# Kernel tuning notes

Measured on AMD Instinct MI355X. Metric: run time of the kernel, lower is better.

Reference implementation:

```python
import jax, jax.numpy as jnp
import numpy as np

SOS = 4998
EOS = 4999
SCALING = 2.0


def setup_inputs() -> dict:
    key = jax.random.key(0)
    ks = jax.random.split(key, 12)
    B, T, E, D, A, C, F, ODIM, L = 32, 1000, 512, 1024, 512, 10, 100, 5000, 100
    s = 0.02
    return {
        "hpad": jax.random.normal(ks[0], (B, T, E), jnp.float32),
        "ys": jax.random.randint(ks[1], (B, L), 0, SOS, jnp.int32),
        # AttLoc params
        "w_enc": jax.random.normal(ks[2], (A, E), jnp.float32) * s,
        "b_enc": jnp.zeros((A,), jnp.float32),
        "w_dec": jax.random.normal(ks[3], (A, D), jnp.float32) * s,
        "w_att": jax.random.normal(ks[4], (A, C), jnp.float32) * s,
        "w_conv": jax.random.normal(ks[5], (C, 1, 2 * F + 1), jnp.float32) * s,  # OIH 1D conv kernel
        "w_gvec": jax.random.normal(ks[6], (1, A), jnp.float32) * s,
        "b_gvec": jnp.zeros((1,), jnp.float32),
        # Decoder params
        "embed": jax.random.normal(ks[7], (ODIM, D), jnp.float32) * s,
        "w_ih": jax.random.normal(ks[8], (4 * D, D + E), jnp.float32) * s,
        "w_hh": jax.random.normal(ks[9], (4 * D, D), jnp.float32) * s,
        "b_ih": jnp.zeros((4 * D,), jnp.float32),
        "b_hh": jnp.zeros((4 * D,), jnp.float32),
        "w_out": jax.random.normal(ks[10], (ODIM, D), jnp.float32) * s,
        "b_out": jnp.zeros((ODIM,), jnp.float32),
    }


def _decode(hpad, ys, w_enc, b_enc, w_dec, w_att, w_conv, w_gvec, b_gvec,
            embed, w_ih, w_hh, b_ih, b_hh, w_out, b_out):
    B, T, E = hpad.shape
    D = w_hh.shape[1]
    F = (w_conv.shape[-1] - 1) // 2
    # ys_in = [sos; y] per utterance (all same length -> already padded)
    ys_in = jnp.concatenate([jnp.full((B, 1), SOS, ys.dtype), ys], axis=1)  # [B, olen]
    eys = embed[ys_in]                                                      # [B, olen, D]
    # pre_compute_enc_h = mlp_enc(enc_h)
    pre = jnp.einsum('bte,ae->bta', hpad, w_enc) + b_enc                    # [B, T, A]
    att0 = jnp.full((B, T), 1.0 / T, hpad.dtype)   # uniform init attention (all hlen == T)
    z0 = jnp.zeros((B, D), hpad.dtype)
    c0 = jnp.zeros((B, D), hpad.dtype)

    def step(carry, ey_i):
        z, c, aw = carry
        # location-aware conv over previous attention weights: [B,1,T] -> [B,C,T]
        conv = jax.lax.conv_general_dilated(aw[:, None, :], w_conv, (1,), [(F, F)],
                                            dimension_numbers=('NCH', 'OIH', 'NCH'))
        att_feat = jnp.einsum('bct,ac->bta', conv, w_att)                   # mlp_att
        dec = (z @ w_dec.T)[:, None, :]                                     # mlp_dec, tiled
        e = jnp.tanh(att_feat + pre + dec) @ w_gvec[0] + b_gvec[0]          # [B, T]
        w = jax.nn.softmax(SCALING * e, axis=1)
        ctx = jnp.einsum('bt,bte->be', w, hpad)                             # [B, E]
        # LSTMCell
        x = jnp.concatenate([ey_i, ctx], axis=1)                            # [B, D+E]
        gates = x @ w_ih.T + b_ih + z @ w_hh.T + b_hh
        i_g, f_g, g_g, o_g = jnp.split(gates, 4, axis=1)
        c_new = jax.nn.sigmoid(f_g) * c + jax.nn.sigmoid(i_g) * jnp.tanh(g_g)
        z_new = jax.nn.sigmoid(o_g) * jnp.tanh(c_new)
        return (z_new, c_new, w), z_new

    _, z_all = jax.lax.scan(step, (z0, c0, att0), jnp.swapaxes(eys, 0, 1))  # [olen, B, D]
    y_all = jnp.einsum('obd,vd->obv', z_all, w_out) + b_out                 # [olen, B, odim]
    return jnp.swapaxes(y_all, 0, 1)                                        # [B, olen, odim]


def reference(hpad, ys, w_enc, b_enc, w_dec, w_att, w_conv, w_gvec, b_gvec,
              embed, w_ih, w_hh, b_ih, b_hh, w_out, b_out):
    return _decode(hpad, ys, w_enc, b_enc, w_dec, w_att, w_conv, w_gvec, b_gvec,
                   embed, w_ih, w_hh, b_ih, b_hh, w_out, b_out)
```

## Files before the change

kernel.cpp:

```cpp
#include <hip/hip_runtime.h>
#include <math.h>

#define B_    32
#define T_    1000
#define E_    512
#define D_    1024
#define A_    512
#define C_    10
#define F_    100
#define ODIM_ 5000
#define OLEN_ 101
#define SOS_  4998

#define OFF_PRE   0u
#define N_PRE     (32u*1000u*512u)
#define OFF_DEC   (OFF_PRE + N_PRE)
#define N_DEC     (32u*512u)
#define OFF_CONV  (OFF_DEC + N_DEC)
#define N_CONVB   (32u*10u*1000u)
#define OFF_EB    (OFF_CONV + N_CONVB)
#define N_EB      (32u*1000u)
#define OFF_AW    (OFF_EB + N_EB)
#define OFF_CTX   (OFF_AW + N_EB)
#define N_CTX     (32u*512u)
#define OFF_GP    (OFF_CTX + N_CTX)
#define N_GP      (10u*32u*4096u)
#define OFF_Z     (OFF_GP + N_GP)
#define N_Z       (32u*1024u)
#define OFF_C     (OFF_Z + N_Z)
#define OFF_ZALL  (OFF_C + N_Z)

__device__ __forceinline__ float fast_tanh(float x) {
    float cx = fminf(8.f, fmaxf(-8.f, x));
    float e = __expf(2.f * cx);
    return (e - 1.f) * __builtin_amdgcn_rcpf(e + 1.f);
}
__device__ __forceinline__ float fast_sigmoid(float x) {
    float cx = fminf(30.f, fmaxf(-30.f, x));
    return __builtin_amdgcn_rcpf(1.f + __expf(-cx));
}

__global__ __launch_bounds__(256) void k_init(float* ws) {
    int i = blockIdx.x * 256 + threadIdx.x;
    if (i < (int)N_Z) { ws[OFF_Z + i] = 0.f; ws[OFF_C + i] = 0.f; }
    if (i < (int)N_EB) ws[OFF_AW + i] = 1.0f / (float)T_;
}

__global__ __launch_bounds__(256) void k_pre(const float* __restrict__ hp,
                                             const float* __restrict__ we,
                                             const float* __restrict__ be,
                                             float* __restrict__ pre) {
    __shared__ float As[64][68];
    __shared__ float Bs[64][68];
    int m0 = blockIdx.y * 64, n0 = blockIdx.x * 64;
    int tid = threadIdx.x;
    int tr = tid >> 4, tc = tid & 15;
    float acc[4][4] = {};
    for (int k0 = 0; k0 < 512; k0 += 64) {
        for (int i = tid; i < 1024; i += 256) {
            int m = i >> 4, kq = (i & 15) << 2;
            float4 v = *(const float4*)&hp[(size_t)(m0 + m) * 512 + k0 + kq];
            As[kq + 0][m] = v.x; As[kq + 1][m] = v.y; As[kq + 2][m] = v.z; As[kq + 3][m] = v.w;
            float4 w = *(const float4*)&we[(size_t)(n0 + m) * 512 + k0 + kq];
            Bs[kq + 0][m] = w.x; Bs[kq + 1][m] = w.y; Bs[kq + 2][m] = w.z; Bs[kq + 3][m] = w.w;
        }
        __syncthreads();
        #pragma unroll 16
        for (int kk = 0; kk < 64; ++kk) {
            float4 av = *(const float4*)&As[kk][tr << 2];
            float4 bv = *(const float4*)&Bs[kk][tc << 2];
            float a[4] = {av.x, av.y, av.z, av.w};
            float b[4] = {bv.x, bv.y, bv.z, bv.w};
            #pragma unroll
            for (int i = 0; i < 4; i++)
                #pragma unroll
                for (int j = 0; j < 4; j++) acc[i][j] += a[i] * b[j];
        }
        __syncthreads();
    }
    #pragma unroll
    for (int i = 0; i < 4; i++) {
        int m = m0 + (tr << 2) + i;
        int n = n0 + (tc << 2);
        float4 o;
        o.x = acc[i][0] + be[n + 0];
        o.y = acc[i][1] + be[n + 1];
        o.z = acc[i][2] + be[n + 2];
        o.w = acc[i][3] + be[n + 3];
        *(float4*)&pre[(size_t)m * 512 + n] = o;
    }
}

__global__ __launch_bounds__(256) void k_prep(const float* __restrict__ wdec,
                                              const float* __restrict__ wconv,
                                              float* ws) {
    int tid = threadIdx.x;
    if (blockIdx.x < 1024) {
        int gw = blockIdx.x * 4 + (tid >> 6);
        int lane = tid & 63;
        int b = gw >> 9, a = gw & 511;
        const float4* wr = (const float4*)(wdec + (size_t)a * 1024);
        const float4* zr = (const float4*)(ws + OFF_Z + b * 1024);
        float acc = 0.f;
        #pragma unroll
        for (int i = 0; i < 4; i++) {
            float4 w4 = wr[i * 64 + lane];
            float4 z4 = zr[i * 64 + lane];
            acc += w4.x * z4.x + w4.y * z4.y + w4.z * z4.z + w4.w * z4.w;
        }
        #pragma unroll
        for (int off = 32; off > 0; off >>= 1) acc += __shfl_xor(acc, off, 64);
        if (lane == 0) ws[OFF_DEC + b * 512 + a] = acc;
    } else {
        int blk = blockIdx.x - 1024;
        int b = blk / 10, c = blk - b * 10;
        if (tid >= 250) return;
        int t = tid * 4;
        const float* ar = ws + OFF_AW + b * 1000;
        const float* wc = wconv + c * 201;
        float a0, a1, a2, a3;
        a0 = (t - 100 >= 0) ? ar[t - 100] : 0.f;
        a1 = (t -  99 >= 0) ? ar[t -  99] : 0.f;
        a2 = (t -  98 >= 0) ? ar[t -  98] : 0.f;
        a3 = (t -  97 >= 0) ? ar[t -  97] : 0.f;
        float c0 = 0.f, c1 = 0.f, c2 = 0.f, c3 = 0.f;
        #pragma unroll 4
        for (int j = 0; j < 201; ++j) {
            float w = wc[j];
            c0 += a0 * w; c1 += a1 * w; c2 += a2 * w; c3 += a3 * w;
            a0 = a1; a1 = a2; a2 = a3;
            int ni = t + j - 96;
            a3 = (ni >= 0 && ni < 1000) ? ar[ni] : 0.f;
        }
        float* o = ws + OFF_CONV + (size_t)(b * 10 + c) * 1000 + t;
        o[0] = c0; o[1] = c1; o[2] = c2; o[3] = c3;
    }
}

__global__ __launch_bounds__(64) void k_energy(const float* __restrict__ watt,
                                               const float* __restrict__ gvec,
                                               const float* __restrict__ bg,
                                               float* ws) {
    int b  = blockIdx.x / 50;
    int t0 = (blockIdx.x - b * 50) * 20;
    int lane = threadIdx.x;
    int a0 = lane * 4, a1 = 256 + lane * 4;
    float wr[8][10];
    #pragma unroll
    for (int i = 0; i < 4; i++)
        #pragma unroll
        for (int c = 0; c < 10; c++) {
            wr[i][c]     = watt[(a0 + i) * 10 + c];
            wr[4 + i][c] = watt[(a1 + i) * 10 + c];
        }
    float4 d0 = *(const float4*)&ws[OFF_DEC + b * 512 + a0];
    float4 d1 = *(const float4*)&ws[OFF_DEC + b * 512 + a1];
    float4 g0 = *(const float4*)&gvec[a0];
    float4 g1 = *(const float4*)&gvec[a1];
    float dc[8] = {d0.x, d0.y, d0.z, d0.w, d1.x, d1.y, d1.z, d1.w};
    float gv[8] = {g0.x, g0.y, g0.z, g0.w, g1.x, g1.y, g1.z, g1.w};
    float bgv = bg[0];
    const float* convb = ws + OFF_CONV + b * 10000;
    for (int it = 0; it < 20; ++it) {
        int t = t0 + it;
        const float* pr = ws + OFF_PRE + (size_t)(b * 1000 + t) * 512;
        float4 p0 = *(const float4*)&pr[a0];
        float4 p1 = *(const float4*)&pr[a1];
        float cv[10];
        #pragma unroll
        for (int c = 0; c < 10; c++) cv[c] = convb[c * 1000 + t];
        float pa[8] = {p0.x, p0.y, p0.z, p0.w, p1.x, p1.y, p1.z, p1.w};
        float acc = 0.f;
        #pragma unroll
        for (int i = 0; i < 8; i++) {
            float s = pa[i] + dc[i];
            #pragma unroll
            for (int c = 0; c < 10; c++) s += cv[c] * wr[i][c];
            acc += gv[i] * fast_tanh(s);
        }
        #pragma unroll
        for (int off = 32; off > 0; off >>= 1) acc += __shfl_xor(acc, off, 64);
        if (lane == 0) ws[OFF_EB + b * 1000 + t] = acc + bgv;
    }
}

__global__ __launch_bounds__(256) void k_softmax(float* ws) {
    int b = blockIdx.x, tid = threadIdx.x;
    ws[OFF_CTX + b * 512 + tid] = 0.f;
    ws[OFF_CTX + b * 512 + 256 + tid] = 0.f;
    __shared__ float red[256];
    const float* e = ws + OFF_EB + b * 1000;
    float s[4];
    float m = -1e30f;
    #pragma unroll
    for (int j = 0; j < 4; j++) {
        int t = tid + j * 256;
        s[j] = (t < 1000) ? 2.0f * e[t] : -1e30f;
        m = fmaxf(m, s[j]);
    }
    red[tid] = m; __syncthreads();
    for (int off = 128; off > 0; off >>= 1) {
        if (tid < off) red[tid] = fmaxf(red[tid], red[tid + off]);
        __syncthreads();
    }
    m = red[0]; __syncthreads();
    float p[4], sum = 0.f;
    #pragma unroll
    for (int j = 0; j < 4; j++) {
        int t = tid + j * 256;
        p[j] = (t < 1000) ? __expf(s[j] - m) : 0.f;
        sum += p[j];
    }
    red[tid] = sum; __syncthreads();
    for (int off = 128; off > 0; off >>= 1) {
        if (tid < off) red[tid] += red[tid + off];
        __syncthreads();
    }
    float inv = __builtin_amdgcn_rcpf(red[0]);
    #pragma unroll
    for (int j = 0; j < 4; j++) {
        int t = tid + j * 256;
        if (t < 1000) ws[OFF_AW + b * 1000 + t] = p[j] * inv;
    }
}

__global__ __launch_bounds__(128) void k_ctx(const float* __restrict__ hp, float* ws) {
    int b = blockIdx.x >> 5, ts = blockIdx.x & 31;
    int e4 = threadIdx.x;
    const float* awr = ws + OFF_AW + b * 1000;
    const float4* hp4 = (const float4*)hp;
    int t0 = ts * 32;
    int t1 = t0 + 32; if (t1 > 1000) t1 = 1000;
    float4 acc = make_float4(0.f, 0.f, 0.f, 0.f);
    for (int t = t0; t < t1; ++t) {
        float w = awr[t];
        float4 h = hp4[(size_t)(b * 1000 + t) * 128 + e4];
        acc.x += w * h.x; acc.y += w * h.y; acc.z += w * h.z; acc.w += w * h.w;
    }
    float* cx = ws + OFF_CTX + b * 512 + e4 * 4;
    atomicAdd(cx + 0, acc.x); atomicAdd(cx + 1, acc.y);
    atomicAdd(cx + 2, acc.z); atomicAdd(cx + 3, acc.w);
}

__global__ __launch_bounds__(128) void k_gates(const float* __restrict__ wih,
                                               const float* __restrict__ whh,
                                               const float* __restrict__ embed,
                                               const int* __restrict__ ys,
                                               float* ws, int step) {
    __shared__ float wlds[32][68];
    __shared__ float xs[32][36];
    int nt = blockIdx.x & 63;
    int ks = blockIdx.x >> 6;
    int n0 = nt * 64;
    int tid = threadIdx.x;
    int nq = tid & 15, bq = tid >> 4;
    float acc[4][4] = {};
    for (int kc = 0; kc < 8; ++kc) {
        int k0 = ks * 256 + kc * 32;
        {
            int r = tid >> 1, h = tid & 1;
            int gn = n0 + r;
            const float* wrow = (k0 < 1536)
                ? (wih + (size_t)gn * 1536 + k0 + h * 16)
                : (whh + (size_t)gn * 1024 + (k0 - 1536) + h * 16);
            #pragma unroll
            for (int j = 0; j < 4; ++j) {
                float4 v = *(const float4*)&wrow[j * 4];
                int kb = h * 16 + j * 4;
                wlds[kb + 0][r] = v.x; wlds[kb + 1][r] = v.y;
                wlds[kb + 2][r] = v.z; wlds[kb + 3][r] = v.w;
            }
        }
        {
            int b = tid >> 2, q = tid & 3;
            int tok = (step == 0) ? SOS_ : ys[b * 100 + step - 1];
            #pragma unroll
            for (int j = 0; j < 2; ++j) {
                int kk = k0 + q * 8 + j * 4;
                float4 v;
                if (kk < 1024)       v = *(const float4*)&embed[(size_t)tok * 1024 + kk];
                else if (kk < 1536)  v = *(const float4*)&ws[OFF_CTX + b * 512 + kk - 1024];
                else                 v = *(const float4*)&ws[OFF_Z + b * 1024 + kk - 1536];
                int kb = q * 8 + j * 4;
                xs[kb + 0][b] = v.x; xs[kb + 1][b] = v.y;
                xs[kb + 2][b] = v.z; xs[kb + 3][b] = v.w;
            }
        }
        __syncthreads();
        #pragma unroll 8
        for (int kk = 0; kk < 32; ++kk) {
            float4 wv = *(const float4*)&wlds[kk][nq * 4];
            float4 xv = *(const float4*)&xs[kk][bq * 4];
            float wa[4] = {wv.x, wv.y, wv.z, wv.w};
            float xa[4] = {xv.x, xv.y, xv.z, xv.w};
            #pragma unroll
            for (int i = 0; i < 4; i++)
                #pragma unroll
                for (int j = 0; j < 4; j++) acc[i][j] += wa[i] * xa[j];
        }
        __syncthreads();
    }
    float* gp = ws + OFF_GP + (size_t)(ks * 32 + bq * 4) * 4096 + n0 + nq * 4;
    #pragma unroll
    for (int j = 0; j < 4; j++)
        #pragma unroll
        for (int i = 0; i < 4; i++)
            gp[(size_t)j * 4096 + i] = acc[i][j];
}

__global__ __launch_bounds__(256) void k_lstm(const float* __restrict__ bih,
                                              const float* __restrict__ bhh,
                                              float* ws, int step) {
    int id = blockIdx.x * 256 + threadIdx.x;
    int b = id >> 10, d = id & 1023;
    float gi = bih[d] + bhh[d];
    float gf = bih[1024 + d] + bhh[1024 + d];
    float gg = bih[2048 + d] + bhh[2048 + d];
    float go = bih[3072 + d] + bhh[3072 + d];
    const float* gp = ws + OFF_GP;
    #pragma unroll
    for (int kc = 0; kc < 10; kc++) {
        const float* r = gp + (size_t)(kc * 32 + b) * 4096;
        gi += r[d];
        gf += r[1024 + d];
        gg += r[2048 + d];
        go += r[3072 + d];
    }
    float c_old = ws[OFF_C + id];
    float si = fast_sigmoid(gi);
    float sf = fast_sigmoid(gf);
    float so = fast_sigmoid(go);
    float cn = sf * c_old + si * fast_tanh(gg);
    float h = so * fast_tanh(cn);
    ws[OFF_C + id] = cn;
    ws[OFF_Z + id] = h;
    ws[OFF_ZALL + ((size_t)step * 32 + b) * 1024 + d] = h;
}

__global__ __launch_bounds__(256) void k_out(const float* __restrict__ zall,
                                             const float* __restrict__ wo,
                                             const float* __restrict__ bo,
                                             float* __restrict__ out) {
    __shared__ float As[64][68];
    __shared__ float Bs[64][68];
    int m0 = blockIdx.y * 64, n0 = blockIdx.x * 64;
    int tid = threadIdx.x;
    int tr = tid >> 4, tc = tid & 15;
    float acc[4][4] = {};
    for (int k0 = 0; k0 < 1024; k0 += 64) {
        for (int i = tid; i < 1024; i += 256) {
            int m = i >> 4, kq = (i & 15) << 2;
            int gm = m0 + m;
            float4 v = (gm < 3232) ? *(const float4*)&zall[(size_t)gm * 1024 + k0 + kq]
                                   : make_float4(0.f, 0.f, 0.f, 0.f);
            As[kq + 0][m] = v.x; As[kq + 1][m] = v.y; As[kq + 2][m] = v.z; As[kq + 3][m] = v.w;
            int gn = n0 + m;
            float4 w = (gn < 5000) ? *(const float4*)&wo[(size_t)gn * 1024 + k0 + kq]
                                   : make_float4(0.f, 0.f, 0.f, 0.f);
            Bs[kq + 0][m] = w.x; Bs[kq + 1][m] = w.y; Bs[kq + 2][m] = w.z; Bs[kq + 3][m] = w.w;
        }
        __syncthreads();
        #pragma unroll 16
        for (int kk = 0; kk < 64; ++kk) {
            float4 av = *(const float4*)&As[kk][tr << 2];
            float4 bv = *(const float4*)&Bs[kk][tc << 2];
            float a[4] = {av.x, av.y, av.z, av.w};
            float b[4] = {bv.x, bv.y, bv.z, bv.w};
            #pragma unroll
            for (int i = 0; i < 4; i++)
                #pragma unroll
                for (int j = 0; j < 4; j++) acc[i][j] += a[i] * b[j];
        }
        __syncthreads();
    }
    #pragma unroll
    for (int i = 0; i < 4; i++) {
        int m = m0 + (tr << 2) + i;
        if (m >= 3232) continue;
        int b = m & 31, o = m >> 5;
        #pragma unroll
        for (int j = 0; j < 4; j++) {
            int v = n0 + (tc << 2) + j;
            if (v < 5000)
                out[((size_t)b * 101 + o) * 5000 + v] = acc[i][j] + bo[v];
        }
    }
}

extern "C" void kernel_launch(void* const* d_in, const int* in_sizes, int n_in,
                              void* d_out, int out_size, void* d_ws, size_t ws_size,
                              hipStream_t stream) {
    const float* hpad   = (const float*)d_in[0];
    const int*   ys     = (const int*)d_in[1];
    const float* w_enc  = (const float*)d_in[2];
    const float* b_enc  = (const float*)d_in[3];
    const float* w_dec  = (const float*)d_in[4];
    const float* w_att  = (const float*)d_in[5];
    const float* w_conv = (const float*)d_in[6];
    const float* w_gvec = (const float*)d_in[7];
    const float* b_gvec = (const float*)d_in[8];
    const float* embed  = (const float*)d_in[9];
    const float* w_ih   = (const float*)d_in[10];
    const float* w_hh   = (const float*)d_in[11];
    const float* b_ih   = (const float*)d_in[12];
    const float* b_hh   = (const float*)d_in[13];
    const float* w_out  = (const float*)d_in[14];
    const float* b_out  = (const float*)d_in[15];
    float* ws  = (float*)d_ws;
    float* out = (float*)d_out;

    k_init<<<128, 256, 0, stream>>>(ws);
    k_pre<<<dim3(8, 500), 256, 0, stream>>>(hpad, w_enc, b_enc, ws + OFF_PRE);

    for (int step = 0; step < OLEN_; ++step) {
        k_prep<<<1024 + 320, 256, 0, stream>>>(w_dec, w_conv, ws);
        k_energy<<<1600, 64, 0, stream>>>(w_att, w_gvec, b_gvec, ws);
        k_softmax<<<32, 256, 0, stream>>>(ws);
        k_ctx<<<1024, 128, 0, stream>>>(hpad, ws);
        k_gates<<<640, 128, 0, stream>>>(w_ih, w_hh, embed, ys, ws, step);
        k_lstm<<<128, 256, 0, stream>>>(b_ih, b_hh, ws, step);
    }

    k_out<<<dim3(79, 51), 256, 0, stream>>>(ws + OFF_ZALL, w_out, b_out, out);
}
```

Measured before the change: 10.91 ms.

## Fuse location conv, energy and softmax numerator into one attention kernel

The location-aware convolution now runs into shared memory inside a new per-(batch, time-chunk) attention kernel, which then computes the energies and their exponentials and atomically accumulates a per-batch sum. Softmax normalisation moves into the context kernel, which reads that sum, writes the normalised weights and uses them directly. The decoder projection becomes its own kernel that keeps each weight row in registers and loops over the batch. This cuts one launch per step and removes the global round trips for the conv output and the energies. In exchange the softmax drops max subtraction, which risks overflow for large energies, and it relies on atomics plus resetting the sum in the LSTM kernel.

```diff
diff --git a/kernel.cpp b/kernel.cpp
--- a/kernel.cpp
+++ b/kernel.cpp
@@ -18,6 +18,7 @@
 #define N_DEC     (32u*512u)
 #define OFF_CONV  (OFF_DEC + N_DEC)
 #define N_CONVB   (32u*10u*1000u)
+#define OFF_SUM   OFF_CONV
 #define OFF_EB    (OFF_CONV + N_CONVB)
 #define N_EB      (32u*1000u)
 #define OFF_AW    (OFF_EB + N_EB)
@@ -44,6 +45,7 @@
     int i = blockIdx.x * 256 + threadIdx.x;
     if (i < (int)N_Z) { ws[OFF_Z + i] = 0.f; ws[OFF_C + i] = 0.f; }
     if (i < (int)N_EB) ws[OFF_AW + i] = 1.0f / (float)T_;
+    if (i < 32) ws[OFF_SUM + i] = 0.f;
 }
 
 __global__ __launch_bounds__(256) void k_pre(const float* __restrict__ hp,
@@ -91,59 +93,55 @@
     }
 }
 
-__global__ __launch_bounds__(256) void k_prep(const float* __restrict__ wdec,
+__global__ __launch_bounds__(256) void k_dec(const float* __restrict__ wdec, float* ws) {
+    int a = blockIdx.x * 4 + (threadIdx.x >> 6);
+    int lane = threadIdx.x & 63;
+    const float4* wr = (const float4*)(wdec + (size_t)a * 1024);
+    float4 w4[4];
+    #pragma unroll
+    for (int j = 0; j < 4; j++) w4[j] = wr[j * 64 + lane];
+    const float4* z4 = (const float4*)(ws + OFF_Z);
+    for (int b = 0; b < 32; ++b) {
+        float acc = 0.f;
+        #pragma unroll
+        for (int j = 0; j < 4; j++) {
+            float4 z = z4[b * 256 + j * 64 + lane];
+            acc += w4[j].x * z.x + w4[j].y * z.y + w4[j].z * z.z + w4[j].w * z.w;
+        }
+        #pragma unroll
+        for (int off = 32; off > 0; off >>= 1) acc += __shfl_xor(acc, off, 64);
+        if (lane == 0) ws[OFF_DEC + b * 512 + a] = acc;
+    }
+}
+
+__global__ __launch_bounds__(512) void k_attn(const float* __restrict__ watt,
+                                              const float* __restrict__ gvec,
+                                              const float* __restrict__ bg,
                                               const float* __restrict__ wconv,
                                               float* ws) {
-    int tid = threadIdx.x;
-    if (blockIdx.x < 1024) {
-        int gw = blockIdx.x * 4 + (tid >> 6);
-        int lane = tid & 63;
-        int b = gw >> 9, a = gw & 511;
-        const float4* wr = (const float4*)(wdec + (size_t)a * 1024);
-        const float4* zr = (const float4*)(ws + OFF_Z + b * 1024);
+    __shared__ float aw_lds[328];
+    __shared__ float conv_lds[10][126];
+    __shared__ float psum;
+    int b  = blockIdx.x >> 3;
+    int tc = blockIdx.x & 7;
+    int t0 = tc * 125;
+    int tid = threadIdx.x;
+    if (tid < 64) ws[OFF_CTX + b * 512 + tc * 64 + tid] = 0.f;
+    if (tid == 0) psum = 0.f;
+    if (tid < 328) {
+        int tg = t0 - 100 + tid;
+        aw_lds[tid] = (tg >= 0 && tg < 1000) ? ws[OFF_AW + b * 1000 + tg] : 0.f;
+    }
+    __syncthreads();
+    for (int i = tid; i < 1250; i += 512) {
+        int c = i / 125, tl = i - c * 125;
+        const float* wc = wconv + c * 201;
         float acc = 0.f;
-        #pragma unroll
-        for (int i = 0; i < 4; i++) {
-            float4 w4 = wr[i * 64 + lane];
-            float4 z4 = zr[i * 64 + lane];
-            acc += w4.x * z4.x + w4.y * z4.y + w4.z * z4.z + w4.w * z4.w;
-        }
-        #pragma unroll
-        for (int off = 32; off > 0; off >>= 1) acc += __shfl_xor(acc, off, 64);
-        if (lane == 0) ws[OFF_DEC + b * 512 + a] = acc;
-    } else {
-        int blk = blockIdx.x - 1024;
-        int b = blk / 10, c = blk - b * 10;
-        if (tid >= 250) return;
-        int t = tid * 4;
-        const float* ar = ws + OFF_AW + b * 1000;
-        const float* wc = wconv + c * 201;
-        float a0, a1, a2, a3;
-        a0 = (t - 100 >= 0) ? ar[t - 100] : 0.f;
-        a1 = (t -  99 >= 0) ? ar[t -  99] : 0.f;
-        a2 = (t -  98 >= 0) ? ar[t -  98] : 0.f;
-        a3 = (t -  97 >= 0) ? ar[t -  97] : 0.f;
-        float c0 = 0.f, c1 = 0.f, c2 = 0.f, c3 = 0.f;
         #pragma unroll 4
-        for (int j = 0; j < 201; ++j) {
-            float w = wc[j];
-            c0 += a0 * w; c1 += a1 * w; c2 += a2 * w; c3 += a3 * w;
-            a0 = a1; a1 = a2; a2 = a3;
-            int ni = t + j - 96;
-            a3 = (ni >= 0 && ni < 1000) ? ar[ni] : 0.f;
-        }
-        float* o = ws + OFF_CONV + (size_t)(b * 10 + c) * 1000 + t;
-        o[0] = c0; o[1] = c1; o[2] = c2; o[3] = c3;
-    }
-}
-
-__global__ __launch_bounds__(64) void k_energy(const float* __restrict__ watt,
-                                               const float* __restrict__ gvec,
-                                               const float* __restrict__ bg,
-                                               float* ws) {
-    int b  = blockIdx.x / 50;
-    int t0 = (blockIdx.x - b * 50) * 20;
-    int lane = threadIdx.x;
+        for (int j = 0; j < 201; ++j) acc += aw_lds[tl + j] * wc[j];
+        conv_lds[c][tl] = acc;
+    }
+    int lane = tid & 63, w = tid >> 6;
     int a0 = lane * 4, a1 = 256 + lane * 4;
     float wr[8][10];
     #pragma unroll
@@ -160,15 +158,17 @@
     float dc[8] = {d0.x, d0.y, d0.z, d0.w, d1.x, d1.y, d1.z, d1.w};
     float gv[8] = {g0.x, g0.y, g0.z, g0.w, g1.x, g1.y, g1.z, g1.w};
     float bgv = bg[0];
-    const float* convb = ws + OFF_CONV + b * 10000;
-    for (int it = 0; it < 20; ++it) {
-        int t = t0 + it;
+    __syncthreads();
+    float lsum = 0.f;
+    int tlo = w * 16, thi = tlo + 16; if (thi > 125) thi = 125;
+    for (int tl = tlo; tl < thi; ++tl) {
+        int t = t0 + tl;
         const float* pr = ws + OFF_PRE + (size_t)(b * 1000 + t) * 512;
         float4 p0 = *(const float4*)&pr[a0];
         float4 p1 = *(const float4*)&pr[a1];
         float cv[10];
         #pragma unroll
-        for (int c = 0; c < 10; c++) cv[c] = convb[c * 1000 + t];
+        for (int c = 0; c < 10; c++) cv[c] = conv_lds[c][tl];
         float pa[8] = {p0.x, p0.y, p0.z, p0.w, p1.x, p1.y, p1.z, p1.w};
         float acc = 0.f;
         #pragma unroll
@@ -180,64 +180,33 @@
         }
         #pragma unroll
         for (int off = 32; off > 0; off >>= 1) acc += __shfl_xor(acc, off, 64);
-        if (lane == 0) ws[OFF_EB + b * 1000 + t] = acc + bgv;
-    }
-}
-
-__global__ __launch_bounds__(256) void k_softmax(float* ws) {
-    int b = blockIdx.x, tid = threadIdx.x;
-    ws[OFF_CTX + b * 512 + tid] = 0.f;
-    ws[OFF_CTX + b * 512 + 256 + tid] = 0.f;
-    __shared__ float red[256];
-    const float* e = ws + OFF_EB + b * 1000;
-    float s[4];
-    float m = -1e30f;
-    #pragma unroll
-    for (int j = 0; j < 4; j++) {
-        int t = tid + j * 256;
-        s[j] = (t < 1000) ? 2.0f * e[t] : -1e30f;
-        m = fmaxf(m, s[j]);
-    }
-    red[tid] = m; __syncthreads();
-    for (int off = 128; off > 0; off >>= 1) {
-        if (tid < off) red[tid] = fmaxf(red[tid], red[tid + off]);
-        __syncthreads();
-    }
-    m = red[0]; __syncthreads();
-    float p[4], sum = 0.f;
-    #pragma unroll
-    for (int j = 0; j < 4; j++) {
-        int t = tid + j * 256;
-        p[j] = (t < 1000) ? __expf(s[j] - m) : 0.f;
-        sum += p[j];
-    }
-    red[tid] = sum; __syncthreads();
-    for (int off = 128; off > 0; off >>= 1) {
-        if (tid < off) red[tid] += red[tid + off];
-        __syncthreads();
-    }
-    float inv = __builtin_amdgcn_rcpf(red[0]);
-    #pragma unroll
-    for (int j = 0; j < 4; j++) {
-        int t = tid + j * 256;
-        if (t < 1000) ws[OFF_AW + b * 1000 + t] = p[j] * inv;
-    }
+        if (lane == 0) {
+            float p = __expf(2.f * (acc + bgv));
+            ws[OFF_EB + b * 1000 + t] = p;
+            lsum += p;
+        }
+    }
+    if (lane == 0) atomicAdd(&psum, lsum);
+    __syncthreads();
+    if (tid == 0) atomicAdd(&ws[OFF_SUM + b], psum);
 }
 
 __global__ __launch_bounds__(128) void k_ctx(const float* __restrict__ hp, float* ws) {
     int b = blockIdx.x >> 5, ts = blockIdx.x & 31;
-    int e4 = threadIdx.x;
-    const float* awr = ws + OFF_AW + b * 1000;
-    const float4* hp4 = (const float4*)hp;
     int t0 = ts * 32;
     int t1 = t0 + 32; if (t1 > 1000) t1 = 1000;
+    int tid = threadIdx.x;
+    float inv = __builtin_amdgcn_rcpf(ws[OFF_SUM + b]);
+    const float* pb = ws + OFF_EB + b * 1000;
+    if (tid < t1 - t0) ws[OFF_AW + b * 1000 + t0 + tid] = pb[t0 + tid] * inv;
+    const float4* hp4 = (const float4*)hp;
     float4 acc = make_float4(0.f, 0.f, 0.f, 0.f);
     for (int t = t0; t < t1; ++t) {
-        float w = awr[t];
-        float4 h = hp4[(size_t)(b * 1000 + t) * 128 + e4];
+        float w = pb[t] * inv;
+        float4 h = hp4[(size_t)(b * 1000 + t) * 128 + tid];
         acc.x += w * h.x; acc.y += w * h.y; acc.z += w * h.z; acc.w += w * h.w;
     }
-    float* cx = ws + OFF_CTX + b * 512 + e4 * 4;
+    float* cx = ws + OFF_CTX + b * 512 + tid * 4;
     atomicAdd(cx + 0, acc.x); atomicAdd(cx + 1, acc.y);
     atomicAdd(cx + 2, acc.z); atomicAdd(cx + 3, acc.w);
 }
@@ -311,6 +280,7 @@
 __global__ __launch_bounds__(256) void k_lstm(const float* __restrict__ bih,
                                               const float* __restrict__ bhh,
                                               float* ws, int step) {
+    if (blockIdx.x == 0 && threadIdx.x < 32) ws[OFF_SUM + threadIdx.x] = 0.f;
     int id = blockIdx.x * 256 + threadIdx.x;
     int b = id >> 10, d = id & 1023;
     float gi = bih[d] + bhh[d];
@@ -413,9 +383,8 @@
     k_pre<<<dim3(8, 500), 256, 0, stream>>>(hpad, w_enc, b_enc, ws + OFF_PRE);
 
     for (int step = 0; step < OLEN_; ++step) {
-        k_prep<<<1024 + 320, 256, 0, stream>>>(w_dec, w_conv, ws);
-        k_energy<<<1600, 64, 0, stream>>>(w_att, w_gvec, b_gvec, ws);
-        k_softmax<<<32, 256, 0, stream>>>(ws);
+        k_dec<<<128, 256, 0, stream>>>(w_dec, ws);
+        k_attn<<<256, 512, 0, stream>>>(w_att, w_gvec, b_gvec, w_conv, ws);
         k_ctx<<<1024, 128, 0, stream>>>(hpad, ws);
         k_gates<<<640, 128, 0, stream>>>(w_ih, w_hh, embed, ys, ws, step);
         k_lstm<<<128, 256, 0, stream>>>(b_ih, b_hh, ws, step);
```

New measurement: 12.43 ms. 1.14x slower.
